# Kernel tuning notes

Hardware: AMD Instinct MI355X
Metric: run time of the kernel (lower is better)

The kernel has to match this reference:

```python
import jax, jax.numpy as jnp
import numpy as np

NUM_HEADS = 16
ROPE_THETA = 10000.0


def apply_rope(x, pos):
    # x: (B, H, S, d_k), pos: (B, S) int
    d = x.shape[-1]
    inv_freq = ROPE_THETA ** (-jnp.arange(0, d, 2, dtype=jnp.float32) / d)  # (d/2,)
    ang = pos[:, None, :, None].astype(jnp.float32) * inv_freq  # (B, 1, S, d/2)
    cos, sin = jnp.cos(ang), jnp.sin(ang)
    x1, x2 = x[..., 0::2], x[..., 1::2]
    even = x1 * cos - x2 * sin
    odd = x1 * sin + x2 * cos
    return jnp.stack([even, odd], axis=-1).reshape(x.shape)


def setup_inputs() -> dict:
    key = jax.random.key(0)
    ks = jax.random.split(key, 5)
    B, S, D = 2, 2048, 1024
    sc = 1.0 / np.sqrt(D)
    return {
        "x": jax.random.normal(ks[0], (B, S, D), dtype=jnp.float32),
        "token_positions": jnp.broadcast_to(jnp.arange(S, dtype=jnp.int32), (B, S)),
        "Wq": jax.random.normal(ks[1], (D, D), dtype=jnp.float32) * sc,
        "Wk": jax.random.normal(ks[2], (D, D), dtype=jnp.float32) * sc,
        "Wv": jax.random.normal(ks[3], (D, D), dtype=jnp.float32) * sc,
        "Wo": jax.random.normal(ks[4], (D, D), dtype=jnp.float32) * sc,
    }


def reference(x, token_positions, Wq, Wk, Wv, Wo):
    B, S, D = x.shape
    H = NUM_HEADS
    dk = D // H
    # bias-free Linear: y = x @ W.T  (W: (out, in))
    def split_heads(t):
        return t.reshape(B, S, H, dk).transpose(0, 2, 1, 3)  # (B, H, S, dk)
    q = split_heads(x @ Wq.T)
    k = split_heads(x @ Wk.T)
    v = split_heads(x @ Wv.T)
    q = apply_rope(q, token_positions)
    k = apply_rope(k, token_positions)
    scores = jnp.einsum("bhqd,bhkd->bhqk", q, k) / jnp.sqrt(jnp.float32(dk))
    causal = jnp.tril(jnp.ones((S, S), dtype=bool))
    scores = jnp.where(causal, scores, jnp.float32(-1e9))
    attn = jax.nn.softmax(scores, axis=-1)
    out = jnp.einsum("bhqk,bhkd->bhqd", attn, v)  # (B, H, S, dk)
    out = out.transpose(0, 2, 1, 3).reshape(B, S, D)
    return out @ Wo.T
```

## Files before the change

### kernel.cpp

```cpp
#include <hip/hip_runtime.h>
#include <math.h>

using bf_t = unsigned short;
typedef short s16x4 __attribute__((ext_vector_type(4)));
typedef short s16x8 __attribute__((ext_vector_type(8)));
typedef float f32x4 __attribute__((ext_vector_type(4)));

__device__ __forceinline__ bf_t f2bf(float f) {
  unsigned u = __float_as_uint(f);
  u += 0x7FFFu + ((u >> 16) & 1u);
  return (bf_t)(u >> 16);
}
__device__ __forceinline__ float bf2f(bf_t h) {
  return __uint_as_float(((unsigned)h) << 16);
}

__device__ __forceinline__ s16x8 ld_frag(const bf_t* p) {
  return *(const s16x8*)p;
}

#define MFMA(A, B, C) __builtin_amdgcn_mfma_f32_16x16x32_bf16((A), (B), (C), 0, 0, 0)

__global__ void cvt_kernel(const float* __restrict__ in, bf_t* __restrict__ out, int n4) {
  int i = blockIdx.x * blockDim.x + threadIdx.x;
  if (i >= n4) return;
  float4 v = ((const float4*)in)[i];
  ushort4 o;
  o.x = f2bf(v.x); o.y = f2bf(v.y); o.z = f2bf(v.z); o.w = f2bf(v.w);
  ((ushort4*)out)[i] = o;
}

template <int EPI>
__global__ __launch_bounds__(256) void gemm_kernel(
    const bf_t* __restrict__ A, const bf_t* __restrict__ Bw,
    float* __restrict__ Cf,
    bf_t* __restrict__ Qb, bf_t* __restrict__ Kb, bf_t* __restrict__ Vt,
    int M, int N, int K) {
  constexpr int BKP = 40;
  __shared__ bf_t As[128 * BKP];
  __shared__ bf_t Bs[128 * BKP];
  const int t = threadIdx.x;
  const int lane = t & 63;
  const int w = t >> 6;
  const int wr = w >> 1, wc = w & 1;
  const int col = lane & 15;
  const int kg = lane >> 4;
  const int m0 = blockIdx.y * 128;
  const int n0 = blockIdx.x * 128;

  f32x4 acc[4][4] = {};

  for (int k0 = 0; k0 < K; k0 += 32) {
#pragma unroll
    for (int p = 0; p < 2; ++p) {
      int idx = t + p * 256;
      int row = idx >> 2;
      int kk = (idx & 3) << 3;
      *(s16x8*)&As[row * BKP + kk] = *(const s16x8*)&A[(size_t)(m0 + row) * K + k0 + kk];
      *(s16x8*)&Bs[row * BKP + kk] = *(const s16x8*)&Bw[(size_t)(n0 + row) * K + k0 + kk];
    }
    __syncthreads();
    s16x8 af[4], bfg[4];
#pragma unroll
    for (int mi = 0; mi < 4; ++mi)
      af[mi] = ld_frag(&As[(wr * 64 + mi * 16 + col) * BKP + kg * 8]);
#pragma unroll
    for (int ni = 0; ni < 4; ++ni)
      bfg[ni] = ld_frag(&Bs[(wc * 64 + ni * 16 + col) * BKP + kg * 8]);
#pragma unroll
    for (int mi = 0; mi < 4; ++mi)
#pragma unroll
      for (int ni = 0; ni < 4; ++ni)
        acc[mi][ni] = MFMA(af[mi], bfg[ni], acc[mi][ni]);
    __syncthreads();
  }

#pragma unroll
  for (int mi = 0; mi < 4; ++mi)
#pragma unroll
    for (int ni = 0; ni < 4; ++ni)
#pragma unroll
      for (int r = 0; r < 4; ++r) {
        int gm = m0 + wr * 64 + mi * 16 + kg * 4 + r;
        int gn = n0 + wc * 64 + ni * 16 + col;
        float v = acc[mi][ni][r];
        if constexpr (EPI == 0) {
          int which = gn >> 10;
          int wn = gn & 1023;
          int h = wn >> 6, d = wn & 63;
          int b = gm >> 11, s = gm & 2047;
          size_t hb = (size_t)(b * 16 + h);
          if (which == 0)
            Qb[(hb * 2048 + s) * 64 + d] = f2bf(v);
          else if (which == 1)
            Kb[(hb * 2048 + s) * 64 + d] = f2bf(v);
          else
            Vt[(hb * 64 + d) * 2048 + s] = f2bf(v);
        } else {
          Cf[(size_t)gm * N + gn] = v;
        }
      }
}

__global__ void rope_kernel(bf_t* __restrict__ Qb, bf_t* __restrict__ Kb,
                            const int* __restrict__ pos, int total) {
  int i = blockIdx.x * blockDim.x + threadIdx.x;
  if (i >= total) return;
  int ip = i & 31;
  int s = (i >> 5) & 2047;
  int bh = i >> 16;
  int b = bh >> 4;
  float p = (float)pos[b * 2048 + s];
  float ang = p * exp2f(-(float)ip * 0.41524101186f);
  float sv, cv;
  sincosf(ang, &sv, &cv);
  size_t base = ((size_t)bh * 2048 + s) * 64 + ip * 2;
  {
    unsigned u = *(const unsigned*)&Qb[base];
    float x1 = bf2f((bf_t)(u & 0xFFFF)), x2 = bf2f((bf_t)(u >> 16));
    unsigned o = (unsigned)f2bf(x1 * cv - x2 * sv) | ((unsigned)f2bf(x1 * sv + x2 * cv) << 16);
    *(unsigned*)&Qb[base] = o;
  }
  {
    unsigned u = *(const unsigned*)&Kb[base];
    float x1 = bf2f((bf_t)(u & 0xFFFF)), x2 = bf2f((bf_t)(u >> 16));
    unsigned o = (unsigned)f2bf(x1 * cv - x2 * sv) | ((unsigned)f2bf(x1 * sv + x2 * cv) << 16);
    *(unsigned*)&Kb[base] = o;
  }
}

__global__ __launch_bounds__(256) void attn_kernel(const bf_t* __restrict__ Qb,
                                                   const bf_t* __restrict__ Kb,
                                                   const bf_t* __restrict__ Vt,
                                                   bf_t* __restrict__ AO) {
  const int t = threadIdx.x;
  const int lane = t & 63;
  const int w = t >> 6;
  const int col = lane & 15;
  const int kg = lane >> 4;
  const int bh = blockIdx.y;
  const int q0 = ((int)gridDim.x - 1 - (int)blockIdx.x) * 64;
  const bf_t* Qp = Qb + (size_t)bh * 2048 * 64;
  const bf_t* Kp = Kb + (size_t)bh * 2048 * 64;
  const bf_t* Vp = Vt + (size_t)bh * 64 * 2048;

  __shared__ char sh[22528];
  bf_t* Plw = (bf_t*)sh + w * 2560;
  float* ocomb = (float*)sh;
  float* mw = (float*)(sh + 20480);
  float* lw = (float*)(sh + 21504);

  s16x8 qf[4][2];
#pragma unroll
  for (int mi = 0; mi < 4; ++mi)
#pragma unroll
    for (int ks = 0; ks < 2; ++ks)
      qf[mi][ks] = ld_frag(Qp + (size_t)(q0 + mi * 16 + col) * 64 + ks * 32 + kg * 8);

  f32x4 o[4][4] = {};
  float mrun[4], lrun[4];
#pragma unroll
  for (int mi = 0; mi < 4; ++mi) {
    mrun[mi] = -INFINITY;
    lrun[mi] = 0.0f;
  }

  for (int kb = w * 32; kb < q0 + 64; kb += 128) {
    s16x8 kf[2][2];
#pragma unroll
    for (int nk = 0; nk < 2; ++nk)
#pragma unroll
      for (int ks = 0; ks < 2; ++ks)
        kf[nk][ks] = ld_frag(Kp + (size_t)(kb + nk * 16 + col) * 64 + ks * 32 + kg * 8);

    f32x4 sc[4][2] = {};
#pragma unroll
    for (int mi = 0; mi < 4; ++mi)
#pragma unroll
      for (int nk = 0; nk < 2; ++nk)
#pragma unroll
        for (int ks = 0; ks < 2; ++ks)
          sc[mi][nk] = MFMA(kf[nk][ks], qf[mi][ks], sc[mi][nk]);

#pragma unroll
    for (int mi = 0; mi < 4; ++mi) {
      const int qg = q0 + mi * 16 + col;
      const int kbase = kb + kg * 4;
      float ev[2][4];
      float mx = -INFINITY;
#pragma unroll
      for (int nk = 0; nk < 2; ++nk)
#pragma unroll
        for (int r = 0; r < 4; ++r) {
          float s = (kbase + nk * 16 + r <= qg) ? sc[mi][nk][r] * 0.125f : -INFINITY;
          ev[nk][r] = s;
          mx = fmaxf(mx, s);
        }
      mx = fmaxf(mx, __shfl_xor(mx, 16));
      mx = fmaxf(mx, __shfl_xor(mx, 32));
      float mold = mrun[mi];
      float mn = fmaxf(mold, mx);
      float mnc = fmaxf(mn, -1e30f);
      float a = __expf(mold - mnc);
      float rs = 0.0f;
#pragma unroll
      for (int nk = 0; nk < 2; ++nk)
#pragma unroll
        for (int r = 0; r < 4; ++r) {
          float e = __expf(ev[nk][r] - mnc);
          ev[nk][r] = e;
          rs += e;
        }
      rs += __shfl_xor(rs, 16);
      rs += __shfl_xor(rs, 32);
      lrun[mi] = lrun[mi] * a + rs;
      mrun[mi] = mn;
#pragma unroll
      for (int ni = 0; ni < 4; ++ni)
#pragma unroll
        for (int r = 0; r < 4; ++r) o[ni][mi][r] *= a;
#pragma unroll
      for (int nk = 0; nk < 2; ++nk) {
        s16x4 p;
        p[0] = (short)f2bf(ev[nk][0]);
        p[1] = (short)f2bf(ev[nk][1]);
        p[2] = (short)f2bf(ev[nk][2]);
        p[3] = (short)f2bf(ev[nk][3]);
        *(s16x4*)&Plw[(mi * 16 + col) * 40 + nk * 16 + kg * 4] = p;
      }
    }

    s16x8 pa[4], vf[4];
#pragma unroll
    for (int mi = 0; mi < 4; ++mi) pa[mi] = ld_frag(&Plw[(mi * 16 + col) * 40 + kg * 8]);
#pragma unroll
    for (int ni = 0; ni < 4; ++ni)
      vf[ni] = ld_frag(Vp + (size_t)(ni * 16 + col) * 2048 + kb + kg * 8);
#pragma unroll
    for (int ni = 0; ni < 4; ++ni)
#pragma unroll
      for (int mi = 0; mi < 4; ++mi) o[ni][mi] = MFMA(vf[ni], pa[mi], o[ni][mi]);
  }

  if (kg == 0) {
#pragma unroll
    for (int mi = 0; mi < 4; ++mi) {
      int row = mi * 16 + col;
      mw[w * 64 + row] = mrun[mi];
      lw[w * 64 + row] = lrun[mi];
    }
  }
  __syncthreads();

  for (int i = t; i < 64 * 65; i += 256) ocomb[i] = 0.0f;
  __syncthreads();

#pragma unroll
  for (int mi = 0; mi < 4; ++mi) {
    int row = mi * 16 + col;
    float ms = fmaxf(fmaxf(mw[row], mw[64 + row]), fmaxf(mw[128 + row], mw[192 + row]));
    float mo = mrun[mi];
    float s = (mo == -INFINITY) ? 0.0f : __expf(mo - ms);
#pragma unroll
    for (int ni = 0; ni < 4; ++ni)
#pragma unroll
      for (int r = 0; r < 4; ++r)
        atomicAdd(&ocomb[row * 65 + ni * 16 + kg * 4 + r], o[ni][mi][r] * s);
  }
  __syncthreads();

  const int b = bh >> 4, h = bh & 15;
#pragma unroll
  for (int r = 0; r < 4; ++r) {
    int row = w * 16 + kg * 4 + r;
    float ms = fmaxf(fmaxf(mw[row], mw[64 + row]), fmaxf(mw[128 + row], mw[192 + row]));
    float ls = 0.0f;
#pragma unroll
    for (int w2 = 0; w2 < 4; ++w2) {
      float mv = mw[w2 * 64 + row];
      ls += (mv == -INFINITY) ? 0.0f : lw[w2 * 64 + row] * __expf(mv - ms);
    }
    float inv = 1.0f / ls;
    int qg = q0 + row;
#pragma unroll
    for (int ni = 0; ni < 4; ++ni)
      AO[((size_t)b * 2048 + qg) * 1024 + h * 64 + ni * 16 + col] =
          f2bf(ocomb[row * 65 + ni * 16 + col] * inv);
  }
}

extern "C" void kernel_launch(void* const* d_in, const int* in_sizes, int n_in,
                              void* d_out, int out_size, void* d_ws, size_t ws_size,
                              hipStream_t stream) {
  const float* x = (const float*)d_in[0];
  const int* pos = (const int*)d_in[1];
  const float* Wq = (const float*)d_in[2];
  const float* Wk = (const float*)d_in[3];
  const float* Wv = (const float*)d_in[4];
  const float* Wo = (const float*)d_in[5];
  float* out = (float*)d_out;

  char* ws = (char*)d_ws;
  bf_t* xb    = (bf_t*)(ws);
  bf_t* Wqkvb = (bf_t*)(ws + 8388608);
  bf_t* Wob   = (bf_t*)(ws + 14680064);
  bf_t* Qb    = (bf_t*)(ws + 16777216);
  bf_t* Kb    = (bf_t*)(ws + 25165824);
  bf_t* Vt    = (bf_t*)(ws + 33554432);
  bf_t* AO    = (bf_t*)(ws + 41943040);

  cvt_kernel<<<4096, 256, 0, stream>>>(x, xb, 1048576);
  cvt_kernel<<<1024, 256, 0, stream>>>(Wq, Wqkvb, 262144);
  cvt_kernel<<<1024, 256, 0, stream>>>(Wk, Wqkvb + 1048576, 262144);
  cvt_kernel<<<1024, 256, 0, stream>>>(Wv, Wqkvb + 2097152, 262144);
  cvt_kernel<<<1024, 256, 0, stream>>>(Wo, Wob, 262144);

  gemm_kernel<0><<<dim3(24, 32), 256, 0, stream>>>(xb, Wqkvb, nullptr, Qb, Kb, Vt,
                                                   4096, 3072, 1024);
  rope_kernel<<<8192, 256, 0, stream>>>(Qb, Kb, pos, 2097152);
  attn_kernel<<<dim3(32, 32), 256, 0, stream>>>(Qb, Kb, Vt, AO);
  gemm_kernel<1><<<dim3(8, 32), 256, 0, stream>>>(AO, Wob, out, nullptr, nullptr, nullptr,
                                                  4096, 1024, 1024);
}
```

Baseline: 341.2 us.

## Prefetch K/V tiles, skip masked blocks, lazy softmax rescale in attention

The 1/sqrt(dk) scale is folded into the RoPE'd Q so the attention loop no longer multiplies scores by it. The attention loop now prefetches the next K tile and loads V at the top of each iteration to overlap global loads with compute. Fully masked 16-row sub-blocks are skipped, and the causal mask is applied only on diagonal tiles. Softmax uses a lazy-rescale path that keeps the running max unless some score exceeds it by more than 8, and it defers the row-sum shuffle reduction to after the loop. This trades extra registers and a wave-wide vote for fewer exp/shuffle operations and fewer idle load stalls.

Result: slower. 406.2 us (+19.1%).

```diff
diff --git a/kernel.cpp b/kernel.cpp
--- a/kernel.cpp
+++ b/kernel.cpp
@@ -118,7 +118,8 @@
   {
     unsigned u = *(const unsigned*)&Qb[base];
     float x1 = bf2f((bf_t)(u & 0xFFFF)), x2 = bf2f((bf_t)(u >> 16));
-    unsigned o = (unsigned)f2bf(x1 * cv - x2 * sv) | ((unsigned)f2bf(x1 * sv + x2 * cv) << 16);
+    unsigned o = (unsigned)f2bf((x1 * cv - x2 * sv) * 0.125f) |
+                 ((unsigned)f2bf((x1 * sv + x2 * cv) * 0.125f) << 16);
     *(unsigned*)&Qb[base] = o;
   }
   {
@@ -165,81 +166,114 @@
     lrun[mi] = 0.0f;
   }
 
-  for (int kb = w * 32; kb < q0 + 64; kb += 128) {
-    s16x8 kf[2][2];
+  const int kend = q0 + 64;
+  const int kb0 = w * 32;
+  s16x8 kf[2][2];
+  if (kb0 < kend) {
 #pragma unroll
     for (int nk = 0; nk < 2; ++nk)
 #pragma unroll
       for (int ks = 0; ks < 2; ++ks)
-        kf[nk][ks] = ld_frag(Kp + (size_t)(kb + nk * 16 + col) * 64 + ks * 32 + kg * 8);
-
-    f32x4 sc[4][2] = {};
-#pragma unroll
-    for (int mi = 0; mi < 4; ++mi)
+        kf[nk][ks] = ld_frag(Kp + (size_t)(kb0 + nk * 16 + col) * 64 + ks * 32 + kg * 8);
+  }
+
+  for (int kb = kb0; kb < kend; kb += 128) {
+    s16x8 vf[4];
+#pragma unroll
+    for (int ni = 0; ni < 4; ++ni)
+      vf[ni] = ld_frag(Vp + (size_t)(ni * 16 + col) * 2048 + kb + kg * 8);
+    const int kbn = kb + 128;
+    s16x8 kfn[2][2];
+    if (kbn < kend) {
 #pragma unroll
       for (int nk = 0; nk < 2; ++nk)
 #pragma unroll
         for (int ks = 0; ks < 2; ++ks)
-          sc[mi][nk] = MFMA(kf[nk][ks], qf[mi][ks], sc[mi][nk]);
+          kfn[nk][ks] = ld_frag(Kp + (size_t)(kbn + nk * 16 + col) * 64 + ks * 32 + kg * 8);
+    }
 
 #pragma unroll
     for (int mi = 0; mi < 4; ++mi) {
+      if (kb > q0 + mi * 16 + 15) continue;
+      f32x4 s0 = {}, s1 = {};
+      s0 = MFMA(kf[0][0], qf[mi][0], s0);
+      s0 = MFMA(kf[0][1], qf[mi][1], s0);
+      s1 = MFMA(kf[1][0], qf[mi][0], s1);
+      s1 = MFMA(kf[1][1], qf[mi][1], s1);
       const int qg = q0 + mi * 16 + col;
-      const int kbase = kb + kg * 4;
-      float ev[2][4];
-      float mx = -INFINITY;
+      if (kb + 31 > q0 + mi * 16) {
+        const int kbase = kb + kg * 4;
+#pragma unroll
+        for (int r = 0; r < 4; ++r) {
+          s0[r] = (kbase + r <= qg) ? s0[r] : -INFINITY;
+          s1[r] = (kbase + 16 + r <= qg) ? s1[r] : -INFINITY;
+        }
+      }
+      float pmax = fmaxf(fmaxf(fmaxf(s0[0], s0[1]), fmaxf(s0[2], s0[3])),
+                         fmaxf(fmaxf(s1[0], s1[1]), fmaxf(s1[2], s1[3])));
+      float m = mrun[mi];
+      if (__all(pmax <= m + 8.0f)) {
+        float mc = fmaxf(m, -1e30f);
+        float rs = 0.0f;
+#pragma unroll
+        for (int r = 0; r < 4; ++r) {
+          s0[r] = __expf(s0[r] - mc);
+          s1[r] = __expf(s1[r] - mc);
+          rs += s0[r] + s1[r];
+        }
+        lrun[mi] += rs;
+      } else {
+        float mx = pmax;
+        mx = fmaxf(mx, __shfl_xor(mx, 16));
+        mx = fmaxf(mx, __shfl_xor(mx, 32));
+        float mn = fmaxf(m, mx);
+        float mnc = fmaxf(mn, -1e30f);
+        float a = __expf(m - mnc);
+        float rs = 0.0f;
+#pragma unroll
+        for (int r = 0; r < 4; ++r) {
+          s0[r] = __expf(s0[r] - mnc);
+          s1[r] = __expf(s1[r] - mnc);
+          rs += s0[r] + s1[r];
+        }
+        lrun[mi] = lrun[mi] * a + rs;
+        mrun[mi] = mn;
+#pragma unroll
+        for (int ni = 0; ni < 4; ++ni)
+#pragma unroll
+          for (int r = 0; r < 4; ++r) o[ni][mi][r] *= a;
+      }
+      s16x4 p0, p1;
+      p0[0] = (short)f2bf(s0[0]); p0[1] = (short)f2bf(s0[1]);
+      p0[2] = (short)f2bf(s0[2]); p0[3] = (short)f2bf(s0[3]);
+      p1[0] = (short)f2bf(s1[0]); p1[1] = (short)f2bf(s1[1]);
+      p1[2] = (short)f2bf(s1[2]); p1[3] = (short)f2bf(s1[3]);
+      *(s16x4*)&Plw[(mi * 16 + col) * 40 + kg * 4] = p0;
+      *(s16x4*)&Plw[(mi * 16 + col) * 40 + 16 + kg * 4] = p1;
+    }
+
+#pragma unroll
+    for (int mi = 0; mi < 4; ++mi) {
+      if (kb > q0 + mi * 16 + 15) continue;
+      s16x8 pa = ld_frag(&Plw[(mi * 16 + col) * 40 + kg * 8]);
+#pragma unroll
+      for (int ni = 0; ni < 4; ++ni) o[ni][mi] = MFMA(vf[ni], pa, o[ni][mi]);
+    }
+
+    if (kbn < kend) {
 #pragma unroll
       for (int nk = 0; nk < 2; ++nk)
 #pragma unroll
-        for (int r = 0; r < 4; ++r) {
-          float s = (kbase + nk * 16 + r <= qg) ? sc[mi][nk][r] * 0.125f : -INFINITY;
-          ev[nk][r] = s;
-          mx = fmaxf(mx, s);
-        }
-      mx = fmaxf(mx, __shfl_xor(mx, 16));
-      mx = fmaxf(mx, __shfl_xor(mx, 32));
-      float mold = mrun[mi];
-      float mn = fmaxf(mold, mx);
-      float mnc = fmaxf(mn, -1e30f);
-      float a = __expf(mold - mnc);
-      float rs = 0.0f;
-#pragma unroll
-      for (int nk = 0; nk < 2; ++nk)
-#pragma unroll
-        for (int r = 0; r < 4; ++r) {
-          float e = __expf(ev[nk][r] - mnc);
-          ev[nk][r] = e;
-          rs += e;
-        }
-      rs += __shfl_xor(rs, 16);
-      rs += __shfl_xor(rs, 32);
-      lrun[mi] = lrun[mi] * a + rs;
-      mrun[mi] = mn;
-#pragma unroll
-      for (int ni = 0; ni < 4; ++ni)
-#pragma unroll
-        for (int r = 0; r < 4; ++r) o[ni][mi][r] *= a;
-#pragma unroll
-      for (int nk = 0; nk < 2; ++nk) {
-        s16x4 p;
-        p[0] = (short)f2bf(ev[nk][0]);
-        p[1] = (short)f2bf(ev[nk][1]);
-        p[2] = (short)f2bf(ev[nk][2]);
-        p[3] = (short)f2bf(ev[nk][3]);
-        *(s16x4*)&Plw[(mi * 16 + col) * 40 + nk * 16 + kg * 4] = p;
-      }
-    }
-
-    s16x8 pa[4], vf[4];
-#pragma unroll
-    for (int mi = 0; mi < 4; ++mi) pa[mi] = ld_frag(&Plw[(mi * 16 + col) * 40 + kg * 8]);
-#pragma unroll
-    for (int ni = 0; ni < 4; ++ni)
-      vf[ni] = ld_frag(Vp + (size_t)(ni * 16 + col) * 2048 + kb + kg * 8);
-#pragma unroll
-    for (int ni = 0; ni < 4; ++ni)
-#pragma unroll
-      for (int mi = 0; mi < 4; ++mi) o[ni][mi] = MFMA(vf[ni], pa[mi], o[ni][mi]);
+        for (int ks = 0; ks < 2; ++ks) kf[nk][ks] = kfn[nk][ks];
+    }
+  }
+
+#pragma unroll
+  for (int mi = 0; mi < 4; ++mi) {
+    float ls = lrun[mi];
+    ls += __shfl_xor(ls, 16);
+    ls += __shfl_xor(ls, 32);
+    lrun[mi] = ls;
   }
 
   if (kg == 0) {
```
